# Kernel optimization log

Measured on AMD Instinct MI355X. Metric: run time of the kernel, lower is better.

## Reference

```python
import jax, jax.numpy as jnp
import numpy as np

EMBED = 1024
HEADS = 16
HEAD_DIM = EMBED // HEADS


def setup_inputs() -> dict:
    key = jax.random.key(0)
    ks = jax.random.split(key, 11)
    B, L, E = 2, 2048, EMBED
    s = 1.0 / np.sqrt(E)
    return {
        "query": jax.random.normal(ks[0], (B, L, E), jnp.float32),
        "key": jax.random.normal(ks[1], (B, L, E), jnp.float32),
        "value": jax.random.normal(ks[2], (B, L, E), jnp.float32),
        "Wq": jax.random.normal(ks[3], (E, E), jnp.float32) * s,
        "bq": jax.random.normal(ks[4], (E,), jnp.float32) * s,
        "Wk": jax.random.normal(ks[5], (E, E), jnp.float32) * s,
        "bk": jax.random.normal(ks[6], (E,), jnp.float32) * s,
        "Wv": jax.random.normal(ks[7], (E, E), jnp.float32) * s,
        "bv": jax.random.normal(ks[8], (E,), jnp.float32) * s,
        "Wo": jax.random.normal(ks[9], (E, E), jnp.float32) * s,
        "bo": jax.random.normal(ks[10], (E,), jnp.float32) * s,
    }


def reference(query, key, value, Wq, bq, Wk, bk, Wv, bv, Wo, bo):
    B, Lq, E = query.shape
    Lk = key.shape[1]
    # Linear projections (torch Linear: x @ W.T + b)
    q = (query @ Wq.T + bq).reshape(B, Lq, HEADS, HEAD_DIM).transpose(0, 2, 1, 3)
    k = (key @ Wk.T + bk).reshape(B, Lk, HEADS, HEAD_DIM).transpose(0, 2, 1, 3)
    v = (value @ Wv.T + bv).reshape(B, Lk, HEADS, HEAD_DIM).transpose(0, 2, 1, 3)
    # NOTE: original scales by sqrt(embed_size), not sqrt(head_dim)
    energy = jnp.einsum("bhqd,bhkd->bhqk", q, k) / jnp.sqrt(jnp.float32(E))
    attn = jax.nn.softmax(energy, axis=-1)
    out = jnp.einsum("bhqk,bhkd->bhqd", attn, v)  # [B,H,Lq,D]
    out = out.transpose(0, 2, 1, 3).reshape(B, Lq, E)
    return out @ Wo.T + bo
```

## Files before the change

### kernel.cpp

```cpp
#include <hip/hip_runtime.h>
#include <hip/hip_bf16.h>


typedef __attribute__((ext_vector_type(4))) float f32x4;
typedef __attribute__((ext_vector_type(16))) float f32x16;
typedef __attribute__((ext_vector_type(8))) short bf16x8;
typedef __attribute__((ext_vector_type(4))) short bf16x4;
typedef __attribute__((ext_vector_type(2))) unsigned int u32x2;

static __device__ __forceinline__ unsigned short f2bf(float f) {
  union { float f; unsigned int u; } a; a.f = f;
  unsigned int u = a.u;
  u += 0x7FFFu + ((u >> 16) & 1u);
  return (unsigned short)(u >> 16);
}

static __device__ __forceinline__ unsigned pack2(float lo, float hi) {
  unsigned a = __float_as_uint(lo) + 0x8000u;
  unsigned b = __float_as_uint(hi) + 0x8000u;
  return __builtin_amdgcn_perm(b, a, 0x07060302);
}

#define AS1(p) ((const __attribute__((address_space(1))) void*)(p))
#define AS3(p) ((__attribute__((address_space(3))) void*)(p))

__global__ __launch_bounds__(256) void cvt_kernel(
    const float* __restrict__ q, const float* __restrict__ k, const float* __restrict__ v,
    const float* __restrict__ wq, const float* __restrict__ wk, const float* __restrict__ wv,
    const float* __restrict__ wo, short* __restrict__ ws) {
  long i = (long)blockIdx.x * 256 + threadIdx.x;
  long e = i * 8;
  const float* src; long off;
  if (e < 12582912) {
    int s = (int)(e >> 22);
    src = s == 0 ? q : (s == 1 ? k : v);
    off = e & 4194303;
  } else {
    long e2 = e - 12582912;
    int s = (int)(e2 >> 20);
    src = s == 0 ? wq : (s == 1 ? wk : (s == 2 ? wv : wo));
    off = e2 & 1048575;
  }
  f32x4 a = *(const f32x4*)(src + off);
  f32x4 b = *(const f32x4*)(src + off + 4);
  bf16x8 o;
  o[0] = (short)f2bf(a[0]); o[1] = (short)f2bf(a[1]);
  o[2] = (short)f2bf(a[2]); o[3] = (short)f2bf(a[3]);
  o[4] = (short)f2bf(b[0]); o[5] = (short)f2bf(b[1]);
  o[6] = (short)f2bf(b[2]); o[7] = (short)f2bf(b[3]);
  *(bf16x8*)(ws + e) = o;
}

__device__ __forceinline__ void gemm_tile(const short* __restrict__ A, const short* __restrict__ B,
                                          int m0, int n0, f32x4 acc[4][4],
                                          short* As, short* Bs) {
  const int t = threadIdx.x;
  const int lane = t & 63, w = t >> 6;
  const int wr = w >> 1, wc = w & 1;
  const int x = lane & 15, g = lane >> 4;
  const int ar = lane >> 2, ac = (lane & 3) * 8;

#pragma unroll
  for (int fm = 0; fm < 4; fm++)
#pragma unroll
    for (int fn = 0; fn < 4; fn++)
#pragma unroll
      for (int r = 0; r < 4; r++) acc[fm][fn][r] = 0.0f;

  for (int k0 = 0; k0 < 1024; k0 += 32) {
    __syncthreads();
#pragma unroll
    for (int i = 0; i < 2; i++) {
      int ch = w * 2 + i;
      const short* ga = A + (long)(m0 + ch * 16 + ar) * 1024 + k0 + ac;
      __builtin_amdgcn_global_load_lds(AS1(ga), AS3(As + ch * 512), 16, 0, 0);
      const short* gb = B + (long)(n0 + ch * 16 + ar) * 1024 + k0 + ac;
      __builtin_amdgcn_global_load_lds(AS1(gb), AS3(Bs + ch * 512), 16, 0, 0);
    }
    __syncthreads();
    bf16x8 af[4], bfv[4];
#pragma unroll
    for (int f = 0; f < 4; f++) {
      af[f]  = *(const bf16x8*)(As + (wr * 64 + f * 16 + x) * 32 + g * 8);
      bfv[f] = *(const bf16x8*)(Bs + (wc * 64 + f * 16 + x) * 32 + g * 8);
    }
#pragma unroll
    for (int fm = 0; fm < 4; fm++)
#pragma unroll
      for (int fn = 0; fn < 4; fn++)
        acc[fm][fn] = __builtin_amdgcn_mfma_f32_16x16x32_bf16(af[fm], bfv[fn], acc[fm][fn], 0, 0, 0);
  }
}

__global__ __launch_bounds__(256) void proj_kernel(
    const short* __restrict__ Xq, const short* __restrict__ Xk, const short* __restrict__ Xv,
    const short* __restrict__ Wq, const short* __restrict__ Wk, const short* __restrict__ Wv,
    const float* __restrict__ bq, const float* __restrict__ bk, const float* __restrict__ bv,
    short* __restrict__ Qo, short* __restrict__ Ko, short* __restrict__ Vto) {
  __shared__ short As[4096], Bs[4096];
  const int z = blockIdx.z;
  const short* A = z == 0 ? Xq : (z == 1 ? Xk : Xv);
  const short* B = z == 0 ? Wq : (z == 1 ? Wk : Wv);
  const float* bias = z == 0 ? bq : (z == 1 ? bk : bv);
  const int m0 = blockIdx.y * 128, n0 = blockIdx.x * 128;
  f32x4 acc[4][4];
  gemm_tile(A, B, m0, n0, acc, As, Bs);

  const int lane = threadIdx.x & 63, w = threadIdx.x >> 6;
  const int wr = w >> 1, wc = w & 1, x = lane & 15, g = lane >> 4;

  if (z == 0) {
    const float scale = 0.04508422002778f;
#pragma unroll
    for (int fn = 0; fn < 4; fn++) {
      int n = n0 + wc * 64 + fn * 16 + x;
      float bb = bias[n];
      int h = n >> 6, d = n & 63;
#pragma unroll
      for (int fm = 0; fm < 4; fm++) {
        int mb = m0 + wr * 64 + fm * 16 + g * 4;
#pragma unroll
        for (int r = 0; r < 4; r++) {
          int m = mb + r;
          int b = m >> 11, l = m & 2047;
          float val = (acc[fm][fn][r] + bb) * scale;
          Qo[((long)((b * 16 + h) * 2048 + l)) * 64 + d] = (short)f2bf(val);
        }
      }
    }
  } else if (z == 1) {
#pragma unroll
    for (int fn = 0; fn < 4; fn++) {
      int n = n0 + wc * 64 + fn * 16 + x;
      float bb = bias[n];
      int h = n >> 6, d = n & 63;
#pragma unroll
      for (int fm = 0; fm < 4; fm++) {
        int mb = m0 + wr * 64 + fm * 16 + g * 4;
#pragma unroll
        for (int r = 0; r < 4; r++) {
          int m = mb + r;
          int b = m >> 11, kv = m & 2047;
          int ds = d ^ ((kv & 7) << 3);
          Ko[((long)((b * 16 + h) * 2048 + kv)) * 64 + ds] = (short)f2bf(acc[fm][fn][r] + bb);
        }
      }
    }
  } else {
#pragma unroll
    for (int fn = 0; fn < 4; fn++) {
      int n = n0 + wc * 64 + fn * 16 + x;
      float bb = bias[n];
      int h = n >> 6, d = n & 63;
#pragma unroll
      for (int fm = 0; fm < 4; fm++) {
        int mb = m0 + wr * 64 + fm * 16 + g * 4;
        int b = mb >> 11, kvb = mb & 2047;
        bf16x4 pk;
#pragma unroll
        for (int r = 0; r < 4; r++) pk[r] = (short)f2bf(acc[fm][fn][r] + bb);
        int kvs = (kvb & ~63) | ((kvb & 63) ^ ((d & 7) << 3));
        *(bf16x4*)(Vto + ((long)((b * 16 + h) * 64 + d)) * 2048 + kvs) = pk;
      }
    }
  }
}

__global__ __launch_bounds__(256, 2) void attn_kernel(
    const short* __restrict__ Qg, const short* __restrict__ Kg,
    const short* __restrict__ Vtg, short* __restrict__ Og) {
  __shared__ __align__(16) short Kl[2][8192];
  __shared__ __align__(16) short Vl[2][8192];
  __shared__ __align__(16) short Pl[4][32][64];
  const int t = threadIdx.x, w = t >> 6, lane = t & 63;
  const int col = lane & 31, hi = lane >> 5;
  const int bh = blockIdx.y;
  const int q0 = blockIdx.x * 128 + w * 32;
  const long hb = (long)bh * 2048 * 64;
  const int swz = (col & 7) * 8;

  bf16x8 qf[4];
#pragma unroll
  for (int ksl = 0; ksl < 4; ksl++)
    qf[ksl] = *(const bf16x8*)(Qg + hb + (long)(q0 + col) * 64 + ksl * 16 + hi * 8);

  f32x16 o0, o1;
#pragma unroll
  for (int i = 0; i < 16; i++) { o0[i] = 0.0f; o1[i] = 0.0f; }
  float l_r = 0.0f;

  auto stage = [&](int buf, int kv0) {
#pragma unroll
    for (int it = 0; it < 4; it++) {
      int cb = it * 256 + w * 64;
      const short* gk = Kg + hb + (long)kv0 * 64 + (cb + lane) * 8;
      __builtin_amdgcn_global_load_lds(AS1(gk), AS3(&Kl[buf][cb * 8]), 16, 0, 0);
      int c = cb + lane;
      const short* gv = Vtg + hb + (long)(c >> 4) * 2048 + kv0 + (c & 15) * 8;
      __builtin_amdgcn_global_load_lds(AS1(gv), AS3(&Vl[buf][cb * 8]), 16, 0, 0);
    }
  };

  stage(0, 0);
  __syncthreads();

  for (int ti = 0; ti < 16; ti++) {
    const int buf = ti & 1;
    if (ti < 15) stage(buf ^ 1, (ti + 1) * 128);

#pragma unroll
    for (int st = 0; st < 2; st++) {
      f32x16 s0, s1;
#pragma unroll
      for (int i = 0; i < 16; i++) { s0[i] = 0.0f; s1[i] = 0.0f; }
      __builtin_amdgcn_s_setprio(1);
#pragma unroll
      for (int ksl = 0; ksl < 4; ksl++) {
        int dcol = (ksl * 16 + hi * 8) ^ swz;
        bf16x8 a0 = *(const bf16x8*)(&Kl[buf][(st * 64 + col) * 64 + dcol]);
        bf16x8 a1 = *(const bf16x8*)(&Kl[buf][(st * 64 + col + 32) * 64 + dcol]);
        s0 = __builtin_amdgcn_mfma_f32_32x32x16_bf16(a0, qf[ksl], s0, 0, 0, 0);
        s1 = __builtin_amdgcn_mfma_f32_32x32x16_bf16(a1, qf[ksl], s1, 0, 0, 0);
      }
      __builtin_amdgcn_s_setprio(0);

#pragma unroll
      for (int i = 0; i < 16; i++) { s0[i] = __builtin_amdgcn_exp2f(s0[i]); }
#pragma unroll
      for (int i = 0; i < 16; i++) { s1[i] = __builtin_amdgcn_exp2f(s1[i]); }
      {
        float a0 = s0[0] + s0[1], a1 = s0[2] + s0[3], a2 = s0[4] + s0[5], a3 = s0[6] + s0[7];
        float a4 = s0[8] + s0[9], a5 = s0[10] + s0[11], a6 = s0[12] + s0[13], a7 = s0[14] + s0[15];
        float b0 = s1[0] + s1[1], b1 = s1[2] + s1[3], b2 = s1[4] + s1[5], b3 = s1[6] + s1[7];
        float b4 = s1[8] + s1[9], b5 = s1[10] + s1[11], b6 = s1[12] + s1[13], b7 = s1[14] + s1[15];
        float c0 = a0 + a1, c1 = a2 + a3, c2 = a4 + a5, c3 = a6 + a7;
        float c4 = b0 + b1, c5 = b2 + b3, c6 = b4 + b5, c7 = b6 + b7;
        float d0 = c0 + c1, d1 = c2 + c3, d2 = c4 + c5, d3 = c6 + c7;
        l_r += (d0 + d1) + (d2 + d3);
      }

#pragma unroll
      for (int j = 0; j < 4; j++) {
        u32x2 p0, p1;
        p0[0] = pack2(s0[4 * j + 0], s0[4 * j + 1]);
        p0[1] = pack2(s0[4 * j + 2], s0[4 * j + 3]);
        int kv = 8 * j + 4 * hi;
        *(u32x2*)&Pl[w][col][kv ^ swz] = p0;
        p1[0] = pack2(s1[4 * j + 0], s1[4 * j + 1]);
        p1[1] = pack2(s1[4 * j + 2], s1[4 * j + 3]);
        *(u32x2*)&Pl[w][col][(32 + kv) ^ swz] = p1;
      }

      __builtin_amdgcn_s_setprio(1);
#pragma unroll
      for (int KS = 0; KS < 4; KS++) {
        const int vcol = (KS * 16 + hi * 8) ^ swz;
        bf16x8 pb  = *(const bf16x8*)&Pl[w][col][vcol];
        bf16x8 vb0 = *(const bf16x8*)(&Vl[buf][col * 128 + st * 64 + vcol]);
        bf16x8 vb1 = *(const bf16x8*)(&Vl[buf][(col + 32) * 128 + st * 64 + vcol]);
        o0 = __builtin_amdgcn_mfma_f32_32x32x16_bf16(vb0, pb, o0, 0, 0, 0);
        o1 = __builtin_amdgcn_mfma_f32_32x32x16_bf16(vb1, pb, o1, 0, 0, 0);
      }
      __builtin_amdgcn_s_setprio(0);
    }

    __syncthreads();
  }

  const float l_tot = l_r + __shfl_xor(l_r, 32);
  const float inv = 1.0f / l_tot;
  const int b = bh >> 4, h = bh & 15;
  const long base = ((long)(b * 2048 + q0 + col) * 16 + h) * 64;
#pragma unroll
  for (int dh = 0; dh < 2; dh++) {
#pragma unroll
    for (int g2 = 0; g2 < 4; g2++) {
      float x0 = (dh ? o1[g2 * 4 + 0] : o0[g2 * 4 + 0]) * inv;
      float x1 = (dh ? o1[g2 * 4 + 1] : o0[g2 * 4 + 1]) * inv;
      float x2 = (dh ? o1[g2 * 4 + 2] : o0[g2 * 4 + 2]) * inv;
      float x3 = (dh ? o1[g2 * 4 + 3] : o0[g2 * 4 + 3]) * inv;
      u32x2 rr;
      rr[0] = (unsigned)f2bf(x0) | ((unsigned)f2bf(x1) << 16);
      rr[1] = (unsigned)f2bf(x2) | ((unsigned)f2bf(x3) << 16);
      int d = dh * 32 + g2 * 8 + hi * 4;
      *(u32x2*)(Og + base + d) = rr;
    }
  }
}

__global__ __launch_bounds__(256) void out_kernel(
    const short* __restrict__ O, const short* __restrict__ Wo,
    const float* __restrict__ bo, float* __restrict__ out) {
  __shared__ short As[4096], Bs[4096];
  const int m0 = blockIdx.y * 128, n0 = blockIdx.x * 128;
  f32x4 acc[4][4];
  gemm_tile(O, Wo, m0, n0, acc, As, Bs);
  const int lane = threadIdx.x & 63, w = threadIdx.x >> 6;
  const int wr = w >> 1, wc = w & 1, x = lane & 15, g = lane >> 4;
#pragma unroll
  for (int fn = 0; fn < 4; fn++) {
    int n = n0 + wc * 64 + fn * 16 + x;
    float bb = bo[n];
#pragma unroll
    for (int fm = 0; fm < 4; fm++) {
      int mb = m0 + wr * 64 + fm * 16 + g * 4;
#pragma unroll
      for (int r = 0; r < 4; r++)
        out[(long)(mb + r) * 1024 + n] = acc[fm][fn][r] + bb;
    }
  }
}

extern "C" void kernel_launch(void* const* d_in, const int* in_sizes, int n_in,
                              void* d_out, int out_size, void* d_ws, size_t ws_size,
                              hipStream_t stream) {
  const float* q  = (const float*)d_in[0];
  const float* k  = (const float*)d_in[1];
  const float* v  = (const float*)d_in[2];
  const float* wq = (const float*)d_in[3];
  const float* bq = (const float*)d_in[4];
  const float* wk = (const float*)d_in[5];
  const float* bk = (const float*)d_in[6];
  const float* wv = (const float*)d_in[7];
  const float* bv = (const float*)d_in[8];
  const float* wo = (const float*)d_in[9];
  const float* bo = (const float*)d_in[10];

  short* ws  = (short*)d_ws;
  short* Xq  = ws;
  short* Xk  = Xq + 4194304;
  short* Xv  = Xk + 4194304;
  short* Wqb = Xv + 4194304;
  short* Wkb = Wqb + 1048576;
  short* Wvb = Wkb + 1048576;
  short* Wob = Wvb + 1048576;
  short* Qb  = Wob + 1048576;
  short* Kb  = Qb + 4194304;
  short* Vtb = Kb + 4194304;
  short* Ob  = Vtb + 4194304;

  cvt_kernel<<<8192, 256, 0, stream>>>(q, k, v, wq, wk, wv, wo, ws);
  dim3 gp(8, 32, 3);
  proj_kernel<<<gp, 256, 0, stream>>>(Xq, Xk, Xv, Wqb, Wkb, Wvb, bq, bk, bv, Qb, Kb, Vtb);
  dim3 ga(16, 32);
  attn_kernel<<<ga, 256, 0, stream>>>(Qb, Kb, Vtb, Ob);
  dim3 gf(8, 32);
  out_kernel<<<gf, 256, 0, stream>>>(Ob, Wob, bo, (float*)d_out);
}
```

Measured before the change: 140.5 us.

## Double GEMM K-step with XOR-swizzled LDS and software-pipeline attention QK^T

The shared GEMM tile now loads a K-slice of 64 per iteration into an XOR-swizzled LDS layout, which halves the number of barrier pairs and avoids LDS bank conflicts on fragment reads. The attention loop is restructured so the QK^T MFMAs for the next sub-tile are issued before the softmax/PV work of the current one, and the first sub-tile of the next KV block is computed right after the barrier. This lets exp and pack work overlap with matrix-core work. The cost is twice the LDS per GEMM block and more live accumulator registers in attention, which may reduce occupancy.

```diff
diff --git a/kernel.cpp b/kernel.cpp
--- a/kernel.cpp
+++ b/kernel.cpp
@@ -58,7 +58,9 @@
   const int lane = t & 63, w = t >> 6;
   const int wr = w >> 1, wc = w & 1;
   const int x = lane & 15, g = lane >> 4;
-  const int ar = lane >> 2, ac = (lane & 3) * 8;
+  const int lr = lane >> 3;
+  const int lc = ((lane & 7) ^ lr) * 8;
+  const int rswz = (x & 7) * 8;
 
 #pragma unroll
   for (int fm = 0; fm < 4; fm++)
@@ -67,28 +69,32 @@
 #pragma unroll
       for (int r = 0; r < 4; r++) acc[fm][fn][r] = 0.0f;
 
-  for (int k0 = 0; k0 < 1024; k0 += 32) {
+  for (int k0 = 0; k0 < 1024; k0 += 64) {
     __syncthreads();
 #pragma unroll
-    for (int i = 0; i < 2; i++) {
-      int ch = w * 2 + i;
-      const short* ga = A + (long)(m0 + ch * 16 + ar) * 1024 + k0 + ac;
+    for (int i = 0; i < 4; i++) {
+      int ch = w * 4 + i;
+      const short* ga = A + (long)(m0 + ch * 8 + lr) * 1024 + k0 + lc;
       __builtin_amdgcn_global_load_lds(AS1(ga), AS3(As + ch * 512), 16, 0, 0);
-      const short* gb = B + (long)(n0 + ch * 16 + ar) * 1024 + k0 + ac;
+      const short* gb = B + (long)(n0 + ch * 8 + lr) * 1024 + k0 + lc;
       __builtin_amdgcn_global_load_lds(AS1(gb), AS3(Bs + ch * 512), 16, 0, 0);
     }
     __syncthreads();
-    bf16x8 af[4], bfv[4];
-#pragma unroll
-    for (int f = 0; f < 4; f++) {
-      af[f]  = *(const bf16x8*)(As + (wr * 64 + f * 16 + x) * 32 + g * 8);
-      bfv[f] = *(const bf16x8*)(Bs + (wc * 64 + f * 16 + x) * 32 + g * 8);
-    }
-#pragma unroll
-    for (int fm = 0; fm < 4; fm++)
-#pragma unroll
-      for (int fn = 0; fn < 4; fn++)
-        acc[fm][fn] = __builtin_amdgcn_mfma_f32_16x16x32_bf16(af[fm], bfv[fn], acc[fm][fn], 0, 0, 0);
+#pragma unroll
+    for (int ks = 0; ks < 2; ks++) {
+      bf16x8 af[4], bfv[4];
+#pragma unroll
+      for (int f = 0; f < 4; f++) {
+        int c = (ks * 32 + g * 8) ^ rswz;
+        af[f]  = *(const bf16x8*)(As + (wr * 64 + f * 16 + x) * 64 + c);
+        bfv[f] = *(const bf16x8*)(Bs + (wc * 64 + f * 16 + x) * 64 + c);
+      }
+#pragma unroll
+      for (int fm = 0; fm < 4; fm++)
+#pragma unroll
+        for (int fn = 0; fn < 4; fn++)
+          acc[fm][fn] = __builtin_amdgcn_mfma_f32_16x16x32_bf16(af[fm], bfv[fn], acc[fm][fn], 0, 0, 0);
+    }
   }
 }
 
@@ -97,7 +103,7 @@
     const short* __restrict__ Wq, const short* __restrict__ Wk, const short* __restrict__ Wv,
     const float* __restrict__ bq, const float* __restrict__ bk, const float* __restrict__ bv,
     short* __restrict__ Qo, short* __restrict__ Ko, short* __restrict__ Vto) {
-  __shared__ short As[4096], Bs[4096];
+  __shared__ short As[8192], Bs[8192];
   const int z = blockIdx.z;
   const short* A = z == 0 ? Xq : (z == 1 ? Xk : Xv);
   const short* B = z == 0 ? Wq : (z == 1 ? Wk : Wv);
@@ -201,70 +207,73 @@
     }
   };
 
+  auto qkt = [&](int buf, int st, f32x16& r0, f32x16& r1) {
+#pragma unroll
+    for (int i = 0; i < 16; i++) { r0[i] = 0.0f; r1[i] = 0.0f; }
+    __builtin_amdgcn_s_setprio(1);
+#pragma unroll
+    for (int ksl = 0; ksl < 4; ksl++) {
+      int dcol = (ksl * 16 + hi * 8) ^ swz;
+      bf16x8 a0 = *(const bf16x8*)(&Kl[buf][(st * 64 + col) * 64 + dcol]);
+      bf16x8 a1 = *(const bf16x8*)(&Kl[buf][(st * 64 + col + 32) * 64 + dcol]);
+      r0 = __builtin_amdgcn_mfma_f32_32x32x16_bf16(a0, qf[ksl], r0, 0, 0, 0);
+      r1 = __builtin_amdgcn_mfma_f32_32x32x16_bf16(a1, qf[ksl], r1, 0, 0, 0);
+    }
+    __builtin_amdgcn_s_setprio(0);
+  };
+
+  auto smpv = [&](int buf, int st, f32x16& s0, f32x16& s1) {
+#pragma unroll
+    for (int i = 0; i < 16; i++) { s0[i] = __builtin_amdgcn_exp2f(s0[i]); }
+#pragma unroll
+    for (int i = 0; i < 16; i++) { s1[i] = __builtin_amdgcn_exp2f(s1[i]); }
+    {
+      float a0 = s0[0] + s0[1], a1 = s0[2] + s0[3], a2 = s0[4] + s0[5], a3 = s0[6] + s0[7];
+      float a4 = s0[8] + s0[9], a5 = s0[10] + s0[11], a6 = s0[12] + s0[13], a7 = s0[14] + s0[15];
+      float b0 = s1[0] + s1[1], b1 = s1[2] + s1[3], b2 = s1[4] + s1[5], b3 = s1[6] + s1[7];
+      float b4 = s1[8] + s1[9], b5 = s1[10] + s1[11], b6 = s1[12] + s1[13], b7 = s1[14] + s1[15];
+      float c0 = a0 + a1, c1 = a2 + a3, c2 = a4 + a5, c3 = a6 + a7;
+      float c4 = b0 + b1, c5 = b2 + b3, c6 = b4 + b5, c7 = b6 + b7;
+      float d0 = c0 + c1, d1 = c2 + c3, d2 = c4 + c5, d3 = c6 + c7;
+      l_r += (d0 + d1) + (d2 + d3);
+    }
+#pragma unroll
+    for (int j = 0; j < 4; j++) {
+      u32x2 p0, p1;
+      p0[0] = pack2(s0[4 * j + 0], s0[4 * j + 1]);
+      p0[1] = pack2(s0[4 * j + 2], s0[4 * j + 3]);
+      int kv = 8 * j + 4 * hi;
+      *(u32x2*)&Pl[w][col][kv ^ swz] = p0;
+      p1[0] = pack2(s1[4 * j + 0], s1[4 * j + 1]);
+      p1[1] = pack2(s1[4 * j + 2], s1[4 * j + 3]);
+      *(u32x2*)&Pl[w][col][(32 + kv) ^ swz] = p1;
+    }
+    __builtin_amdgcn_s_setprio(1);
+#pragma unroll
+    for (int KS = 0; KS < 4; KS++) {
+      const int vcol = (KS * 16 + hi * 8) ^ swz;
+      bf16x8 pb  = *(const bf16x8*)&Pl[w][col][vcol];
+      bf16x8 vb0 = *(const bf16x8*)(&Vl[buf][col * 128 + st * 64 + vcol]);
+      bf16x8 vb1 = *(const bf16x8*)(&Vl[buf][(col + 32) * 128 + st * 64 + vcol]);
+      o0 = __builtin_amdgcn_mfma_f32_32x32x16_bf16(vb0, pb, o0, 0, 0, 0);
+      o1 = __builtin_amdgcn_mfma_f32_32x32x16_bf16(vb1, pb, o1, 0, 0, 0);
+    }
+    __builtin_amdgcn_s_setprio(0);
+  };
+
   stage(0, 0);
   __syncthreads();
 
+  f32x16 cur0, cur1, nxt0, nxt1;
+  qkt(0, 0, cur0, cur1);
   for (int ti = 0; ti < 16; ti++) {
     const int buf = ti & 1;
     if (ti < 15) stage(buf ^ 1, (ti + 1) * 128);
-
-#pragma unroll
-    for (int st = 0; st < 2; st++) {
-      f32x16 s0, s1;
-#pragma unroll
-      for (int i = 0; i < 16; i++) { s0[i] = 0.0f; s1[i] = 0.0f; }
-      __builtin_amdgcn_s_setprio(1);
-#pragma unroll
-      for (int ksl = 0; ksl < 4; ksl++) {
-        int dcol = (ksl * 16 + hi * 8) ^ swz;
-        bf16x8 a0 = *(const bf16x8*)(&Kl[buf][(st * 64 + col) * 64 + dcol]);
-        bf16x8 a1 = *(const bf16x8*)(&Kl[buf][(st * 64 + col + 32) * 64 + dcol]);
-        s0 = __builtin_amdgcn_mfma_f32_32x32x16_bf16(a0, qf[ksl], s0, 0, 0, 0);
-        s1 = __builtin_amdgcn_mfma_f32_32x32x16_bf16(a1, qf[ksl], s1, 0, 0, 0);
-      }
-      __builtin_amdgcn_s_setprio(0);
-
-#pragma unroll
-      for (int i = 0; i < 16; i++) { s0[i] = __builtin_amdgcn_exp2f(s0[i]); }
-#pragma unroll
-      for (int i = 0; i < 16; i++) { s1[i] = __builtin_amdgcn_exp2f(s1[i]); }
-      {
-        float a0 = s0[0] + s0[1], a1 = s0[2] + s0[3], a2 = s0[4] + s0[5], a3 = s0[6] + s0[7];
-        float a4 = s0[8] + s0[9], a5 = s0[10] + s0[11], a6 = s0[12] + s0[13], a7 = s0[14] + s0[15];
-        float b0 = s1[0] + s1[1], b1 = s1[2] + s1[3], b2 = s1[4] + s1[5], b3 = s1[6] + s1[7];
-        float b4 = s1[8] + s1[9], b5 = s1[10] + s1[11], b6 = s1[12] + s1[13], b7 = s1[14] + s1[15];
-        float c0 = a0 + a1, c1 = a2 + a3, c2 = a4 + a5, c3 = a6 + a7;
-        float c4 = b0 + b1, c5 = b2 + b3, c6 = b4 + b5, c7 = b6 + b7;
-        float d0 = c0 + c1, d1 = c2 + c3, d2 = c4 + c5, d3 = c6 + c7;
-        l_r += (d0 + d1) + (d2 + d3);
-      }
-
-#pragma unroll
-      for (int j = 0; j < 4; j++) {
-        u32x2 p0, p1;
-        p0[0] = pack2(s0[4 * j + 0], s0[4 * j + 1]);
-        p0[1] = pack2(s0[4 * j + 2], s0[4 * j + 3]);
-        int kv = 8 * j + 4 * hi;
-        *(u32x2*)&Pl[w][col][kv ^ swz] = p0;
-        p1[0] = pack2(s1[4 * j + 0], s1[4 * j + 1]);
-        p1[1] = pack2(s1[4 * j + 2], s1[4 * j + 3]);
-        *(u32x2*)&Pl[w][col][(32 + kv) ^ swz] = p1;
-      }
-
-      __builtin_amdgcn_s_setprio(1);
-#pragma unroll
-      for (int KS = 0; KS < 4; KS++) {
-        const int vcol = (KS * 16 + hi * 8) ^ swz;
-        bf16x8 pb  = *(const bf16x8*)&Pl[w][col][vcol];
-        bf16x8 vb0 = *(const bf16x8*)(&Vl[buf][col * 128 + st * 64 + vcol]);
-        bf16x8 vb1 = *(const bf16x8*)(&Vl[buf][(col + 32) * 128 + st * 64 + vcol]);
-        o0 = __builtin_amdgcn_mfma_f32_32x32x16_bf16(vb0, pb, o0, 0, 0, 0);
-        o1 = __builtin_amdgcn_mfma_f32_32x32x16_bf16(vb1, pb, o1, 0, 0, 0);
-      }
-      __builtin_amdgcn_s_setprio(0);
-    }
-
+    qkt(buf, 1, nxt0, nxt1);
+    smpv(buf, 0, cur0, cur1);
+    smpv(buf, 1, nxt0, nxt1);
     __syncthreads();
+    if (ti < 15) qkt(buf ^ 1, 0, cur0, cur1);
   }
 
   const float l_tot = l_r + __shfl_xor(l_r, 32);
@@ -291,7 +300,7 @@
 __global__ __launch_bounds__(256) void out_kernel(
     const short* __restrict__ O, const short* __restrict__ Wo,
     const float* __restrict__ bo, float* __restrict__ out) {
-  __shared__ short As[4096], Bs[4096];
+  __shared__ short As[8192], Bs[8192];
   const int m0 = blockIdx.y * 128, n0 = blockIdx.x * 128;
   f32x4 acc[4][4];
   gemm_tile(O, Wo, m0, n0, acc, As, Bs);
```

Result: faster. 136.5 us (-2.9%).
